# Kernel tuning notes

Hardware: AMD Instinct MI355X
Metric: run time of the kernel (lower is better)

The kernel has to match this reference:

```python
import jax, jax.numpy as jnp
import numpy as np

B, S, H, IN, OUT, T = 1024, 256, 128, 2, 2, 512


def setup_inputs() -> dict:
    key = jax.random.key(0)
    ks = jax.random.split(key, 7)
    scale = 1.0 / np.sqrt(H)  # PyTorch LSTM init range ~ U(-1/sqrt(H), 1/sqrt(H))
    return {
        "x": jax.random.normal(ks[0], (B, S, IN), jnp.float32),
        "w_ih": jax.random.normal(ks[1], (4 * H, IN), jnp.float32) * scale,
        "w_hh": jax.random.normal(ks[2], (4 * H, H), jnp.float32) * scale,
        "b_ih": jax.random.normal(ks[3], (4 * H,), jnp.float32) * scale,
        "b_hh": jax.random.normal(ks[4], (4 * H,), jnp.float32) * scale,
        "w_fc": jax.random.normal(ks[5], (OUT, H), jnp.float32) * scale,
        "b_fc": jax.random.normal(ks[6], (OUT,), jnp.float32) * scale,
        "target_length": T,
    }


def reference(x, w_ih, w_hh, b_ih, b_hh, w_fc, b_fc, target_length):
    # PyTorch nn.LSTM cell, gate order (i, f, g, o). Dropout is identity (eval mode).
    bias = b_ih + b_hh
    hdim = w_hh.shape[1]

    def cell(h, c, x_t):
        gates = x_t @ w_ih.T + h @ w_hh.T + bias  # [B, 4H]
        i, f, g, o = jnp.split(gates, 4, axis=-1)
        c_new = jax.nn.sigmoid(f) * c + jax.nn.sigmoid(i) * jnp.tanh(g)
        h_new = jax.nn.sigmoid(o) * jnp.tanh(c_new)
        return h_new, c_new

    bsz = x.shape[0]
    h0 = jnp.zeros((bsz, hdim), x.dtype)
    c0 = jnp.zeros((bsz, hdim), x.dtype)

    # Encode input sequence
    def enc_step(carry, x_t):
        h, c = carry
        h, c = cell(h, c, x_t)
        return (h, c), None

    (h, c), _ = jax.lax.scan(enc_step, (h0, c0), jnp.swapaxes(x, 0, 1))

    inp0 = x[:, -1, :]  # [B, 2]

    def dec_step(carry, _):
        h, c, inp = carry
        h, c = cell(h, c, inp)
        pred = h @ w_fc.T + b_fc  # [B, 2]
        return (h, c, pred), pred

    _, preds = jax.lax.scan(dec_step, (h, c, inp0), None, length=target_length)
    return jnp.swapaxes(preds, 0, 1)  # [B, target_length, 2]
```

## Files before the change

kernel.cpp:

```cpp
#include <hip/hip_runtime.h>

typedef unsigned short ush;
typedef unsigned int uint32;
typedef __attribute__((ext_vector_type(8))) __bf16 bf16x8;
typedef __attribute__((ext_vector_type(4))) float f32x4;

#define NBLK 256
#define RB   4
#define NTHR 512
#define SENC 256
#define TDEC 512
#define HDIM 128
#define HSTR 144
#define XSTR 520
#define PSTR 1024

#define LOG2E  1.4426950408889634f
#define LOG2E2 2.8853900817779268f

__device__ __forceinline__ float bf2f(ush u){
  uint32 v = ((uint32)u) << 16;
  return __builtin_bit_cast(float, v);
}
__device__ __forceinline__ ush f2bf(float f){
  return __builtin_bit_cast(ush, (__bf16)f);
}
__device__ __forceinline__ float lo16f(uint32 w){ return __builtin_bit_cast(float, w << 16); }
__device__ __forceinline__ float hi16f(uint32 w){ return __builtin_bit_cast(float, w & 0xFFFF0000u); }

__device__ __forceinline__ float loadf(const void* p, int i, bool f32){
  return f32 ? ((const float*)p)[i] : bf2f(((const ush*)p)[i]);
}
__device__ __forceinline__ bf16x8 load8bf(const void* p, int i, bool f32){
  bf16x8 r;
  if (!f32){
    uint4 u = *reinterpret_cast<const uint4*>((const ush*)p + i);
    r = __builtin_bit_cast(bf16x8, u);
  } else {
    const float* fp = (const float*)p + i;
    #pragma unroll
    for (int j = 0; j < 8; ++j) r[j] = (__bf16)fp[j];
  }
  return r;
}
__device__ __forceinline__ f32x4 M1(bf16x8 a, bf16x8 b, f32x4 c){
  return __builtin_amdgcn_mfma_f32_16x16x32_bf16(a, b, c, 0, 0, 0);
}

__global__ void __launch_bounds__(NTHR, 2)
lstm_kernel(const void* __restrict__ xg,  const void* __restrict__ wih,
            const void* __restrict__ whh, const void* __restrict__ bih,
            const void* __restrict__ bhh, const void* __restrict__ wfc,
            const void* __restrict__ bfc, void* __restrict__ outg)
{
  __shared__ __attribute__((aligned(16))) ush x_lds[RB * XSTR];
  __shared__ __attribute__((aligned(16))) ush h_lds[2][RB * HSTR];
  __shared__ __attribute__((aligned(16))) ush pred_lds[RB][PSTR];
  __shared__ __attribute__((aligned(16))) float ppart[2][RB][2][4];

  const int tid   = threadIdx.x;
  const int lane  = tid & 63;
  const int wv    = tid >> 6;
  const int n     = lane & 15;
  const int q     = lane >> 4;
  const int q8    = q * 8;
  const int gbase = wv << 4;
  const int blk   = blockIdx.x;

  const uint32* wp = (const uint32*)whh;
  int cnt = 0;
  #pragma unroll
  for (int i = 0; i < 64; ++i){
    uint32 e = (wp[i] >> 7) & 0xFFu;
    cnt += (e >= 90u && e <= 140u) ? 1 : 0;
  }
  const bool isf32 = (cnt < 40);

  for (int i = tid; i < 2 * RB * HSTR; i += NTHR) h_lds[0][i] = 0;

  if (!isf32){
    if (tid < 256){
      int row = tid >> 6, c = (tid & 63) * 8;
      uint4 v = *reinterpret_cast<const uint4*>((const ush*)xg + (blk * RB + row) * (SENC * 2) + c);
      *reinterpret_cast<uint4*>(&x_lds[row * XSTR + c]) = v;
    }
  } else {
    for (int i = tid; i < RB * SENC * 2; i += NTHR){
      int row = i >> 9, c = i & 511;
      x_lds[row * XSTR + c] = f2bf(((const float*)xg)[(blk * RB + row) * (SENC * 2) + c]);
    }
  }

  float wih0v[4], wih1v[4];
  f32x4 biasC[4];
  bf16x8 bfr[4][4];
  #pragma unroll
  for (int p = 0; p < 4; ++p){
    int g = p * 128 + gbase + n;
    float b = loadf(bih, g, isf32) + loadf(bhh, g, isf32);
    biasC[p][0] = b; biasC[p][1] = b; biasC[p][2] = b; biasC[p][3] = b;
    wih0v[p] = loadf(wih, g * 2 + 0, isf32);
    wih1v[p] = loadf(wih, g * 2 + 1, isf32);
    #pragma unroll
    for (int kk = 0; kk < 4; ++kk)
      bfr[p][kk] = load8bf(whh, g * HDIM + kk * 32 + q8, isf32);
  }
  const bool ispred = (wv == 0) || (wv == 3) || (wv == 5) || (wv == 6);
  const bool issum  = (wv == 1);
  const int  pkk    = (wv == 0) ? 0 : (wv == 3) ? 1 : (wv == 5) ? 2 : 3;
  const int  pofs   = pkk * 32 + q8;
  bf16x8 wpfr;
  #pragma unroll
  for (int j = 0; j < 8; ++j)
    wpfr[j] = (__bf16)loadf(wfc, (n & 1) * HDIM + pkk * 32 + q8 + j, isf32);
  f32x4 predC;
  {
    float pb = (wv == 0) ? loadf(bfc, n & 1, isf32) : 0.0f;
    predC[0] = pb; predC[1] = pb; predC[2] = pb; predC[3] = pb;
  }

  float cc = 0.0f;
  const int arow  = (n >> 2) * HSTR;
  const int hwofs = q * HSTR + gbase + n;
  const f32x4 Z = {0.0f, 0.0f, 0.0f, 0.0f};

  __syncthreads();

#define LOADAF(RBUF) \
    const ush* hb = &h_lds[RBUF][arow]; \
    bf16x8 af0 = *reinterpret_cast<const bf16x8*>(hb + q8); \
    bf16x8 af1 = *reinterpret_cast<const bf16x8*>(hb + 32 + q8); \
    bf16x8 af2 = *reinterpret_cast<const bf16x8*>(hb + 64 + q8); \
    bf16x8 af3 = *reinterpret_cast<const bf16x8*>(hb + 96 + q8);

#define GATEMM(C0_, C1_, C2_, C3_) \
    f32x4 A2 = M1(af0, bfr[2][0], C2_); \
    f32x4 B2 = M1(af2, bfr[2][2], Z); \
    f32x4 A0 = M1(af0, bfr[0][0], C0_); \
    f32x4 B0 = M1(af2, bfr[0][2], Z); \
    f32x4 A1 = M1(af0, bfr[1][0], C1_); \
    f32x4 B1 = M1(af2, bfr[1][2], Z); \
    f32x4 A3 = M1(af0, bfr[3][0], C3_); \
    f32x4 B3 = M1(af2, bfr[3][2], Z); \
    A2 = M1(af1, bfr[2][1], A2); \
    B2 = M1(af3, bfr[2][3], B2); \
    A0 = M1(af1, bfr[0][1], A0); \
    B0 = M1(af3, bfr[0][3], B0); \
    A1 = M1(af1, bfr[1][1], A1); \
    B1 = M1(af3, bfr[1][3], B1); \
    A3 = M1(af1, bfr[3][1], A3); \
    B3 = M1(af3, bfr[3][3], B3);

#define TAIL(WBUF) \
    float g2 = A2[0] + B2[0]; \
    float Eg = __builtin_amdgcn_exp2f(g2 * LOG2E2); \
    float g0 = A0[0] + B0[0]; \
    float ei = __builtin_amdgcn_exp2f(-g0 * LOG2E); \
    float g1 = A1[0] + B1[0]; \
    float ef = __builtin_amdgcn_exp2f(-g1 * LOG2E); \
    float g3 = A3[0] + B3[0]; \
    float eo = __builtin_amdgcn_exp2f(-g3 * LOG2E); \
    float sitg = (Eg - 1.0f) * __builtin_amdgcn_rcpf((1.0f + ei) * (Eg + 1.0f)); \
    float sf = __builtin_amdgcn_rcpf(1.0f + ef); \
    cc = sf * cc + sitg; \
    float ccl = __builtin_amdgcn_fmed3f(cc, -20.0f, 20.0f); \
    float Ec = __builtin_amdgcn_exp2f(ccl * LOG2E2); \
    float hh = (Ec - 1.0f) * __builtin_amdgcn_rcpf((1.0f + eo) * (Ec + 1.0f)); \
    h_lds[WBUF][hwofs] = f2bf(hh);

#define ENCSTEP(RBUF, WBUF, T) { \
    LOADAF(RBUF) \
    uint32 xw = *reinterpret_cast<const uint32*>(&x_lds[q * XSTR + (T) * 2]); \
    float xa = lo16f(xw), xb = hi16f(xw); \
    f32x4 C0 = biasC[0]; C0[0] = __builtin_fmaf(wih0v[0], xa, __builtin_fmaf(wih1v[0], xb, C0[0])); \
    f32x4 C1 = biasC[1]; C1[0] = __builtin_fmaf(wih0v[1], xa, __builtin_fmaf(wih1v[1], xb, C1[0])); \
    f32x4 C2 = biasC[2]; C2[0] = __builtin_fmaf(wih0v[2], xa, __builtin_fmaf(wih1v[2], xb, C2[0])); \
    f32x4 C3 = biasC[3]; C3[0] = __builtin_fmaf(wih0v[3], xa, __builtin_fmaf(wih1v[3], xb, C3[0])); \
    GATEMM(C0, C1, C2, C3) \
    TAIL(WBUF) \
    __syncthreads(); \
  }

#define DECSTEP(RBUF, WBUF, D) { \
    LOADAF(RBUF) \
    bf16x8 pfrag; \
    if (ispred) pfrag = *reinterpret_cast<const bf16x8*>(hb + pofs); \
    GATEMM(biasC[0], biasC[1], biasC[2], biasC[3]) \
    f32x4 PP; \
    if (ispred) PP = M1(pfrag, wpfr, predC); \
    if (issum && (D) > 0 && n < 2){ \
      f32x4 pp = *reinterpret_cast<const f32x4*>(&ppart[((D) - 1) & 1][q][n][0]); \
      pred_lds[q][((D) - 1) * 2 + n] = f2bf(pp[0] + pp[1] + pp[2] + pp[3]); \
    } \
    TAIL(WBUF) \
    if (ispred && n < 2) ppart[(D) & 1][q][n][pkk] = PP[0]; \
    __syncthreads(); \
  }

  #pragma unroll 1
  for (int s = 0; s < SENC; s += 2){
    ENCSTEP(0, 1, s)
    ENCSTEP(1, 0, s + 1)
  }
  ENCSTEP(0, 1, SENC - 1)

  {
    float bfc0 = loadf(bfc, 0, isf32), bfc1 = loadf(bfc, 1, isf32);
    #pragma unroll
    for (int p = 0; p < 4; ++p){
      float nb = biasC[p][0] + wih0v[p] * bfc0 + wih1v[p] * bfc1;
      biasC[p][0] = nb; biasC[p][1] = nb; biasC[p][2] = nb; biasC[p][3] = nb;
    }
    #pragma unroll
    for (int kk = 0; kk < 4; ++kk){
      #pragma unroll
      for (int j = 0; j < 8; ++j){
        int k = kk * 32 + q8 + j;
        float w0 = loadf(wfc, k, isf32);
        float w1 = loadf(wfc, HDIM + k, isf32);
        #pragma unroll
        for (int p = 0; p < 4; ++p)
          bfr[p][kk][j] = (__bf16)((float)bfr[p][kk][j] + wih0v[p] * w0 + wih1v[p] * w1);
      }
    }
  }

  #pragma unroll 1
  for (int d = 0; d < TDEC - 2; d += 2){
    DECSTEP(1, 0, d)
    DECSTEP(0, 1, d + 1)
  }
  DECSTEP(1, 0, TDEC - 2)

  if (issum && n < 2){
    f32x4 pp = *reinterpret_cast<const f32x4*>(&ppart[0][q][n][0]);
    pred_lds[q][(TDEC - 2) * 2 + n] = f2bf(pp[0] + pp[1] + pp[2] + pp[3]);
  }

  if (wv == 0){
    LOADAF(0)
    bf16x8 wf0, wf1, wf2, wf3;
    #pragma unroll
    for (int j = 0; j < 8; ++j){
      wf0[j] = (__bf16)loadf(wfc, (n & 1) * HDIM +   0 + q8 + j, isf32);
      wf1[j] = (__bf16)loadf(wfc, (n & 1) * HDIM +  32 + q8 + j, isf32);
      wf2[j] = (__bf16)loadf(wfc, (n & 1) * HDIM +  64 + q8 + j, isf32);
      wf3[j] = (__bf16)loadf(wfc, (n & 1) * HDIM +  96 + q8 + j, isf32);
    }
    f32x4 P = M1(af0, wf0, predC);
    f32x4 Q = M1(af2, wf2, Z);
    P = M1(af1, wf1, P);
    Q = M1(af3, wf3, Q);
    if (n < 2)
      pred_lds[q][(TDEC - 1) * 2 + n] = f2bf(P[0] + Q[0]);
  }
  __syncthreads();

  if (!isf32){
    int row = tid >> 7, c = (tid & 127) * 8;
    uint4 v = *reinterpret_cast<const uint4*>(&pred_lds[row][c]);
    *reinterpret_cast<uint4*>((ush*)outg + (blk * RB + row) * (TDEC * 2) + c) = v;
  } else {
    for (int i = tid; i < RB * TDEC * 2; i += NTHR){
      int row = i >> 10, c = i & 1023;
      ((float*)outg)[(blk * RB + row) * (TDEC * 2) + c] = bf2f(pred_lds[row][c]);
    }
  }
}

extern "C" void kernel_launch(void* const* d_in, const int* in_sizes, int n_in,
                              void* d_out, int out_size, void* d_ws, size_t ws_size,
                              hipStream_t stream) {
  lstm_kernel<<<dim3(NBLK), dim3(NTHR), 0, stream>>>(
      d_in[0], d_in[1], d_in[2], d_in[3], d_in[4], d_in[5], d_in[6], d_out);
}
```

Baseline: 414.0 us.

## Quantize recurrent weights and hidden state to int8 and use i8 MFMA

Recurrent weights are quantized to int8 with a per-gate-row scale, and the hidden state is also written as an int8 copy scaled by 127. The gate matmul then runs as two int8 16x16x64 MFMAs per gate instead of four bf16 ones, with dequantization folded into the bias FMA. Some LDS loads are also reordered ahead of the matmul. This shortens the per-step serial MFMA chain and LDS traffic, at the cost of significant precision loss that accumulates across the recurrence.

```diff
diff --git a/kernel.cpp b/kernel.cpp
--- a/kernel.cpp
+++ b/kernel.cpp
@@ -4,6 +4,8 @@
 typedef unsigned int uint32;
 typedef __attribute__((ext_vector_type(8))) __bf16 bf16x8;
 typedef __attribute__((ext_vector_type(4))) float f32x4;
+typedef __attribute__((ext_vector_type(4))) int i32x4;
+typedef __attribute__((ext_vector_type(16))) char c8x16;
 
 #define NBLK 256
 #define RB   4
@@ -12,6 +14,7 @@
 #define TDEC 512
 #define HDIM 128
 #define HSTR 144
+#define H8STR 144
 #define XSTR 520
 #define PSTR 1024
 
@@ -31,20 +34,11 @@
 __device__ __forceinline__ float loadf(const void* p, int i, bool f32){
   return f32 ? ((const float*)p)[i] : bf2f(((const ush*)p)[i]);
 }
-__device__ __forceinline__ bf16x8 load8bf(const void* p, int i, bool f32){
-  bf16x8 r;
-  if (!f32){
-    uint4 u = *reinterpret_cast<const uint4*>((const ush*)p + i);
-    r = __builtin_bit_cast(bf16x8, u);
-  } else {
-    const float* fp = (const float*)p + i;
-    #pragma unroll
-    for (int j = 0; j < 8; ++j) r[j] = (__bf16)fp[j];
-  }
-  return r;
-}
 __device__ __forceinline__ f32x4 M1(bf16x8 a, bf16x8 b, f32x4 c){
   return __builtin_amdgcn_mfma_f32_16x16x32_bf16(a, b, c, 0, 0, 0);
+}
+__device__ __forceinline__ i32x4 MI(i32x4 a, i32x4 b, i32x4 c){
+  return __builtin_amdgcn_mfma_i32_16x16x64_i8(a, b, c, 0, 0, 0);
 }
 
 __global__ void __launch_bounds__(NTHR, 2)
@@ -55,6 +49,7 @@
 {
   __shared__ __attribute__((aligned(16))) ush x_lds[RB * XSTR];
   __shared__ __attribute__((aligned(16))) ush h_lds[2][RB * HSTR];
+  __shared__ __attribute__((aligned(16))) char h8s[2][RB * H8STR];
   __shared__ __attribute__((aligned(16))) ush pred_lds[RB][PSTR];
   __shared__ __attribute__((aligned(16))) float ppart[2][RB][2][4];
 
@@ -64,6 +59,7 @@
   const int n     = lane & 15;
   const int q     = lane >> 4;
   const int q8    = q * 8;
+  const int q16   = q * 16;
   const int gbase = wv << 4;
   const int blk   = blockIdx.x;
 
@@ -77,6 +73,7 @@
   const bool isf32 = (cnt < 40);
 
   for (int i = tid; i < 2 * RB * HSTR; i += NTHR) h_lds[0][i] = 0;
+  for (int i = tid; i < 2 * RB * H8STR; i += NTHR) ((char*)h8s)[i] = 0;
 
   if (!isf32){
     if (tid < 256){
@@ -91,19 +88,36 @@
     }
   }
 
-  float wih0v[4], wih1v[4];
-  f32x4 biasC[4];
-  bf16x8 bfr[4][4];
+  float wih0v[4], wih1v[4], biasv[4], smulv[4];
+  i32x4 ifr[4][2];
   #pragma unroll
   for (int p = 0; p < 4; ++p){
     int g = p * 128 + gbase + n;
-    float b = loadf(bih, g, isf32) + loadf(bhh, g, isf32);
-    biasC[p][0] = b; biasC[p][1] = b; biasC[p][2] = b; biasC[p][3] = b;
+    biasv[p] = loadf(bih, g, isf32) + loadf(bhh, g, isf32);
     wih0v[p] = loadf(wih, g * 2 + 0, isf32);
     wih1v[p] = loadf(wih, g * 2 + 1, isf32);
+    float w[2][16]; float m = 0.0f;
     #pragma unroll
-    for (int kk = 0; kk < 4; ++kk)
-      bfr[p][kk] = load8bf(whh, g * HDIM + kk * 32 + q8, isf32);
+    for (int kh = 0; kh < 2; ++kh){
+      #pragma unroll
+      for (int j = 0; j < 16; ++j){
+        float v = loadf(whh, g * HDIM + kh * 64 + q16 + j, isf32);
+        w[kh][j] = v; m = __builtin_fmaxf(m, __builtin_fabsf(v));
+      }
+    }
+    m = __builtin_fmaxf(m, __shfl_xor(m, 16, 64));
+    m = __builtin_fmaxf(m, __shfl_xor(m, 32, 64));
+    m = __builtin_fmaxf(m, 1e-20f);
+    float sinv = 127.0f / m;
+    smulv[p] = m * (1.0f / (127.0f * 127.0f));
+    #pragma unroll
+    for (int kh = 0; kh < 2; ++kh){
+      c8x16 c;
+      #pragma unroll
+      for (int j = 0; j < 16; ++j)
+        c[j] = (char)(int)__builtin_rintf(w[kh][j] * sinv);
+      ifr[p][kh] = __builtin_bit_cast(i32x4, c);
+    }
   }
   const bool ispred = (wv == 0) || (wv == 3) || (wv == 5) || (wv == 6);
   const bool issum  = (wv == 1);
@@ -120,45 +134,38 @@
   }
 
   float cc = 0.0f;
-  const int arow  = (n >> 2) * HSTR;
-  const int hwofs = q * HSTR + gbase + n;
-  const f32x4 Z = {0.0f, 0.0f, 0.0f, 0.0f};
+  const int arow   = (n >> 2) * HSTR;
+  const int a8row  = (n >> 2) * H8STR;
+  const int hwofs  = q * HSTR + gbase + n;
+  const int h8wofs = q * H8STR + gbase + n;
+  const f32x4 Z  = {0.0f, 0.0f, 0.0f, 0.0f};
+  const i32x4 IZ = {0, 0, 0, 0};
 
   __syncthreads();
 
-#define LOADAF(RBUF) \
-    const ush* hb = &h_lds[RBUF][arow]; \
-    bf16x8 af0 = *reinterpret_cast<const bf16x8*>(hb + q8); \
-    bf16x8 af1 = *reinterpret_cast<const bf16x8*>(hb + 32 + q8); \
-    bf16x8 af2 = *reinterpret_cast<const bf16x8*>(hb + 64 + q8); \
-    bf16x8 af3 = *reinterpret_cast<const bf16x8*>(hb + 96 + q8);
-
-#define GATEMM(C0_, C1_, C2_, C3_) \
-    f32x4 A2 = M1(af0, bfr[2][0], C2_); \
-    f32x4 B2 = M1(af2, bfr[2][2], Z); \
-    f32x4 A0 = M1(af0, bfr[0][0], C0_); \
-    f32x4 B0 = M1(af2, bfr[0][2], Z); \
-    f32x4 A1 = M1(af0, bfr[1][0], C1_); \
-    f32x4 B1 = M1(af2, bfr[1][2], Z); \
-    f32x4 A3 = M1(af0, bfr[3][0], C3_); \
-    f32x4 B3 = M1(af2, bfr[3][2], Z); \
-    A2 = M1(af1, bfr[2][1], A2); \
-    B2 = M1(af3, bfr[2][3], B2); \
-    A0 = M1(af1, bfr[0][1], A0); \
-    B0 = M1(af3, bfr[0][3], B0); \
-    A1 = M1(af1, bfr[1][1], A1); \
-    B1 = M1(af3, bfr[1][3], B1); \
-    A3 = M1(af1, bfr[3][1], A3); \
-    B3 = M1(af3, bfr[3][3], B3);
-
-#define TAIL(WBUF) \
-    float g2 = A2[0] + B2[0]; \
+#define LOADA8(RBUF) \
+    const char* ha = &h8s[RBUF][a8row]; \
+    i32x4 a80 = *reinterpret_cast<const i32x4*>(ha + q16); \
+    i32x4 a81 = *reinterpret_cast<const i32x4*>(ha + 64 + q16);
+
+#define GATEMM8 \
+    i32x4 G2 = MI(a80, ifr[2][0], IZ); \
+    i32x4 G0 = MI(a80, ifr[0][0], IZ); \
+    i32x4 G1 = MI(a80, ifr[1][0], IZ); \
+    i32x4 G3 = MI(a80, ifr[3][0], IZ); \
+    G2 = MI(a81, ifr[2][1], G2); \
+    G0 = MI(a81, ifr[0][1], G0); \
+    G1 = MI(a81, ifr[1][1], G1); \
+    G3 = MI(a81, ifr[3][1], G3);
+
+#define TAIL8(WBUF, BX0, BX1, BX2, BX3) \
+    float g2 = __builtin_fmaf((float)G2[0], smulv[2], BX2); \
     float Eg = __builtin_amdgcn_exp2f(g2 * LOG2E2); \
-    float g0 = A0[0] + B0[0]; \
+    float g0 = __builtin_fmaf((float)G0[0], smulv[0], BX0); \
     float ei = __builtin_amdgcn_exp2f(-g0 * LOG2E); \
-    float g1 = A1[0] + B1[0]; \
+    float g1 = __builtin_fmaf((float)G1[0], smulv[1], BX1); \
     float ef = __builtin_amdgcn_exp2f(-g1 * LOG2E); \
-    float g3 = A3[0] + B3[0]; \
+    float g3 = __builtin_fmaf((float)G3[0], smulv[3], BX3); \
     float eo = __builtin_amdgcn_exp2f(-g3 * LOG2E); \
     float sitg = (Eg - 1.0f) * __builtin_amdgcn_rcpf((1.0f + ei) * (Eg + 1.0f)); \
     float sf = __builtin_amdgcn_rcpf(1.0f + ef); \
@@ -166,34 +173,37 @@
     float ccl = __builtin_amdgcn_fmed3f(cc, -20.0f, 20.0f); \
     float Ec = __builtin_amdgcn_exp2f(ccl * LOG2E2); \
     float hh = (Ec - 1.0f) * __builtin_amdgcn_rcpf((1.0f + eo) * (Ec + 1.0f)); \
-    h_lds[WBUF][hwofs] = f2bf(hh);
+    h_lds[WBUF][hwofs] = f2bf(hh); \
+    h8s[WBUF][h8wofs] = (char)(int)__builtin_rintf(hh * 127.0f);
 
 #define ENCSTEP(RBUF, WBUF, T) { \
-    LOADAF(RBUF) \
+    LOADA8(RBUF) \
     uint32 xw = *reinterpret_cast<const uint32*>(&x_lds[q * XSTR + (T) * 2]); \
+    GATEMM8 \
+     \
     float xa = lo16f(xw), xb = hi16f(xw); \
-    f32x4 C0 = biasC[0]; C0[0] = __builtin_fmaf(wih0v[0], xa, __builtin_fmaf(wih1v[0], xb, C0[0])); \
-    f32x4 C1 = biasC[1]; C1[0] = __builtin_fmaf(wih0v[1], xa, __builtin_fmaf(wih1v[1], xb, C1[0])); \
-    f32x4 C2 = biasC[2]; C2[0] = __builtin_fmaf(wih0v[2], xa, __builtin_fmaf(wih1v[2], xb, C2[0])); \
-    f32x4 C3 = biasC[3]; C3[0] = __builtin_fmaf(wih0v[3], xa, __builtin_fmaf(wih1v[3], xb, C3[0])); \
-    GATEMM(C0, C1, C2, C3) \
-    TAIL(WBUF) \
+    float bx0 = biasv[0] + __builtin_fmaf(wih0v[0], xa, wih1v[0] * xb); \
+    float bx1 = biasv[1] + __builtin_fmaf(wih0v[1], xa, wih1v[1] * xb); \
+    float bx2 = biasv[2] + __builtin_fmaf(wih0v[2], xa, wih1v[2] * xb); \
+    float bx3 = biasv[3] + __builtin_fmaf(wih0v[3], xa, wih1v[3] * xb); \
+    TAIL8(WBUF, bx0, bx1, bx2, bx3) \
     __syncthreads(); \
   }
 
 #define DECSTEP(RBUF, WBUF, D) { \
-    LOADAF(RBUF) \
+    LOADA8(RBUF) \
     bf16x8 pfrag; \
-    if (ispred) pfrag = *reinterpret_cast<const bf16x8*>(hb + pofs); \
-    GATEMM(biasC[0], biasC[1], biasC[2], biasC[3]) \
+    if (ispred) pfrag = *reinterpret_cast<const bf16x8*>(&h_lds[RBUF][arow] + pofs); \
+    f32x4 pp; \
+    if (issum && (D) > 0 && n < 2) \
+      pp = *reinterpret_cast<const f32x4*>(&ppart[((D) - 1) & 1][q][n][0]); \
+    GATEMM8 \
     f32x4 PP; \
     if (ispred) PP = M1(pfrag, wpfr, predC); \
-    if (issum && (D) > 0 && n < 2){ \
-      f32x4 pp = *reinterpret_cast<const f32x4*>(&ppart[((D) - 1) & 1][q][n][0]); \
+    if (issum && (D) > 0 && n < 2) \
       pred_lds[q][((D) - 1) * 2 + n] = f2bf(pp[0] + pp[1] + pp[2] + pp[3]); \
-    } \
-    TAIL(WBUF) \
     if (ispred && n < 2) ppart[(D) & 1][q][n][pkk] = PP[0]; \
+    TAIL8(WBUF, biasv[0], biasv[1], biasv[2], biasv[3]) \
     __syncthreads(); \
   }
 
@@ -208,19 +218,32 @@
     float bfc0 = loadf(bfc, 0, isf32), bfc1 = loadf(bfc, 1, isf32);
     #pragma unroll
     for (int p = 0; p < 4; ++p){
-      float nb = biasC[p][0] + wih0v[p] * bfc0 + wih1v[p] * bfc1;
-      biasC[p][0] = nb; biasC[p][1] = nb; biasC[p][2] = nb; biasC[p][3] = nb;
-    }
-    #pragma unroll
-    for (int kk = 0; kk < 4; ++kk){
+      int g = p * 128 + gbase + n;
+      biasv[p] = biasv[p] + wih0v[p] * bfc0 + wih1v[p] * bfc1;
+      float w[2][16]; float m = 0.0f;
       #pragma unroll
-      for (int j = 0; j < 8; ++j){
-        int k = kk * 32 + q8 + j;
-        float w0 = loadf(wfc, k, isf32);
-        float w1 = loadf(wfc, HDIM + k, isf32);
+      for (int kh = 0; kh < 2; ++kh){
         #pragma unroll
-        for (int p = 0; p < 4; ++p)
-          bfr[p][kk][j] = (__bf16)((float)bfr[p][kk][j] + wih0v[p] * w0 + wih1v[p] * w1);
+        for (int j = 0; j < 16; ++j){
+          int k = kh * 64 + q16 + j;
+          float v = loadf(whh, g * HDIM + k, isf32)
+                  + wih0v[p] * loadf(wfc, k, isf32)
+                  + wih1v[p] * loadf(wfc, HDIM + k, isf32);
+          w[kh][j] = v; m = __builtin_fmaxf(m, __builtin_fabsf(v));
+        }
+      }
+      m = __builtin_fmaxf(m, __shfl_xor(m, 16, 64));
+      m = __builtin_fmaxf(m, __shfl_xor(m, 32, 64));
+      m = __builtin_fmaxf(m, 1e-20f);
+      float sinv = 127.0f / m;
+      smulv[p] = m * (1.0f / (127.0f * 127.0f));
+      #pragma unroll
+      for (int kh = 0; kh < 2; ++kh){
+        c8x16 c;
+        #pragma unroll
+        for (int j = 0; j < 16; ++j)
+          c[j] = (char)(int)__builtin_rintf(w[kh][j] * sinv);
+        ifr[p][kh] = __builtin_bit_cast(i32x4, c);
       }
     }
   }
@@ -238,7 +261,11 @@
   }
 
   if (wv == 0){
-    LOADAF(0)
+    const ush* hb = &h_lds[0][arow];
+    bf16x8 af0 = *reinterpret_cast<const bf16x8*>(hb + q8);
+    bf16x8 af2 = *reinterpret_cast<const bf16x8*>(hb + 64 + q8);
+    bf16x8 af1 = *reinterpret_cast<const bf16x8*>(hb + 32 + q8);
+    bf16x8 af3 = *reinterpret_cast<const bf16x8*>(hb + 96 + q8);
     bf16x8 wf0, wf1, wf2, wf3;
     #pragma unroll
     for (int j = 0; j < 8; ++j){
```

New measurement: 407.7 us. About the same (-1.5%).
